# Performance work log

Hardware: AMD Instinct MI355X
Metric: run time of the kernel (lower is better)

## Reference

```python
import jax, jax.numpy as jnp
import numpy as np
from jax import lax

# physiological constants from the source module
DT = 1.0
TAU_L = 10.0
G_B = 0.6
G_L = 1.0 / TAU_L
LAMBDA_MAX = 0.35
STEPS = int(50 / DT)

IN_SIZE, HID, OUT, BATCH = 1024, 2048, 512, 4096


def setup_inputs() -> dict:
    key = jax.random.key(0)
    k1, k2, k3, k4, k5, k6 = jax.random.split(key, 6)
    psp = jax.random.uniform(k1, (IN_SIZE, BATCH), dtype=jnp.float32)  # |mm(spikes,kernel)| is >=0
    label = jax.random.uniform(k2, (BATCH, OUT), dtype=jnp.float32)    # teaching current I
    # Linear params init: uniform(-0.1, 0.1) as in the torch module
    W_h = jax.random.uniform(k3, (HID, IN_SIZE), minval=-0.1, maxval=0.1, dtype=jnp.float32)
    b_h = jax.random.uniform(k4, (HID,), minval=-0.1, maxval=0.1, dtype=jnp.float32)
    W_o = jax.random.uniform(k5, (OUT, HID), minval=-0.1, maxval=0.1, dtype=jnp.float32)
    b_o = jax.random.uniform(k6, (OUT,), minval=-0.1, maxval=0.1, dtype=jnp.float32)
    return {"psp": psp, "label": label, "W_h": W_h, "b_h": b_h, "W_o": W_o, "b_o": b_o}


def reference(psp, label, W_h, b_h, W_o, b_o):
    a = DT / TAU_L
    gr = G_B / G_L  # = 6.0
    x = psp.T  # [B, in] -- Hidden_layer transposes basal_input
    # psp is constant over the time loop, so the hidden basal GEMM hoists out
    basal_V_h = x @ W_h.T + b_h  # [B, HID]
    soma_h0 = jnp.zeros_like(basal_V_h)
    soma_o0 = jnp.zeros((x.shape[0], W_o.shape[0]), dtype=x.dtype)

    def step(carry, _):
        soma_h, soma_o = carry
        # hidden two-compartment leaky integration
        soma_h = soma_h + a * (-soma_h + gr * (basal_V_h - soma_h))
        rate_h = LAMBDA_MAX * jax.nn.sigmoid(soma_h)  # [B, HID]
        basal_V_o = rate_h @ W_o.T + b_o              # [B, OUT]
        # output layer, training (test=False) branch: nudged by teaching current I=label
        soma_o = soma_o + a * (-soma_o + gr * (basal_V_o - soma_o) + label - soma_o)
        return (soma_h, soma_o), None

    (soma_h, soma_o), _ = lax.scan(step, (soma_h0, soma_o0), None, length=STEPS)
    return LAMBDA_MAX * jax.nn.sigmoid(soma_o)  # out_layer.spike_rate, [B, OUT]
```

## Files before the change

kernel.cpp:

```cpp
#include <hip/hip_runtime.h>
#include <hip/hip_bf16.h>


typedef __bf16 bf16_t;
typedef __bf16 bf16x8 __attribute__((ext_vector_type(8)));
typedef __bf16 bf16x4v __attribute__((ext_vector_type(4)));
typedef float f32x4 __attribute__((ext_vector_type(4)));

#define GLD_TO_LDS16(gp, lp)                                            \
  __builtin_amdgcn_global_load_lds(                                     \
      (__attribute__((address_space(1))) void*)(void*)(gp),             \
      (__attribute__((address_space(3))) void*)(lp), 16, 0, 0)

__global__ __launch_bounds__(256) void transpose_cvt(
    const float* __restrict__ in, bf16_t* __restrict__ out, int R, int C) {
  __shared__ float tile[64][65];
  const int tx = threadIdx.x & 63;
  const int ty = threadIdx.x >> 6;
  const int r0 = blockIdx.y * 64;
  const int c0 = blockIdx.x * 64;
#pragma unroll
  for (int i = 0; i < 16; ++i) {
    const int r = ty + i * 4;
    tile[r][tx] = in[(size_t)(r0 + r) * C + c0 + tx];
  }
  __syncthreads();
#pragma unroll
  for (int i = 0; i < 16; ++i) {
    const int r = ty + i * 4;
    out[(size_t)(c0 + r) * R + r0 + tx] = (bf16_t)tile[tx][r];
  }
}

__global__ __launch_bounds__(256) void cvt2_f32_bf16(
    const float4* __restrict__ w1, bf16x4v* __restrict__ o1, int n1,
    const float4* __restrict__ w2, bf16x4v* __restrict__ o2, int n2) {
  const int i = blockIdx.x * 256 + threadIdx.x;
  const float4 v = (i < n1) ? w1[i] : w2[i - n1];
  bf16x4v o;
  o.x = (bf16_t)v.x; o.y = (bf16_t)v.y; o.z = (bf16_t)v.z; o.w = (bf16_t)v.w;
  if (i < n1) o1[i] = o;
  else if (i - n1 < n2) o2[i - n1] = o;
}

__global__ __launch_bounds__(256, 4) void gemm1_nt(
    const bf16_t* __restrict__ A, const bf16_t* __restrict__ Bt,
    const float* __restrict__ bias, bf16_t* __restrict__ C,
    int M, int N, int K) {
  constexpr int BK = 64;
  __shared__ __align__(16) bf16_t sA[128 * BK];
  __shared__ __align__(16) bf16_t sB[64 * BK];

  const int tid = threadIdx.x;
  const int wave = tid >> 6;
  const int lane = tid & 63;
  const int bm = blockIdx.x * 128;
  const int bn = blockIdx.y * 64;
  const int wm = (wave & 1) * 64;
  const int wn = (wave >> 1) * 32;

  f32x4 acc[4][2] = {};

  const int srow8 = lane >> 3;
  const int gseg = (lane & 7) ^ srow8;
  const bf16_t* Ag = A + (size_t)(bm + wave * 32 + srow8) * K + gseg * 8;
  const bf16_t* Bg = Bt + (size_t)(bn + wave * 16 + srow8) * K + gseg * 8;
  const int dstA = wave * 2048;
  const int dstB = wave * 1024;

  const int fr = lane & 15;
  const int qh = lane >> 4;

  for (int k0 = 0; k0 < K; k0 += BK) {
#pragma unroll
    for (int c = 0; c < 4; ++c)
      GLD_TO_LDS16(Ag + (size_t)(c * 8) * K + k0, sA + dstA + c * 512);
#pragma unroll
    for (int c = 0; c < 2; ++c)
      GLD_TO_LDS16(Bg + (size_t)(c * 8) * K + k0, sB + dstB + c * 512);
    __syncthreads();

#pragma unroll
    for (int ks = 0; ks < 2; ++ks) {
      const int q = ks * 4 + qh;
      bf16x8 av[4], bv[2];
#pragma unroll
      for (int i = 0; i < 4; ++i) {
        const int rr = wm + i * 16 + fr;
        av[i] = *(const bf16x8*)(sA + rr * BK + ((q ^ (rr & 7)) * 8));
      }
#pragma unroll
      for (int j = 0; j < 2; ++j) {
        const int rr = wn + j * 16 + fr;
        bv[j] = *(const bf16x8*)(sB + rr * BK + ((q ^ (rr & 7)) * 8));
      }
#pragma unroll
      for (int i = 0; i < 4; ++i)
#pragma unroll
        for (int j = 0; j < 2; ++j)
          acc[i][j] = __builtin_amdgcn_mfma_f32_16x16x32_bf16(
              av[i], bv[j], acc[i][j], 0, 0, 0);
    }
    __syncthreads();
  }

  const int cm0 = (lane >> 4) * 4;
#pragma unroll
  for (int j = 0; j < 2; ++j) {
    const int gn = bn + wn + j * 16 + fr;
    const float bj = bias[gn];
#pragma unroll
    for (int i = 0; i < 4; ++i) {
#pragma unroll
      for (int r = 0; r < 4; ++r) {
        const int gm = bm + wm + i * 16 + cm0 + r;
        const float z = 0.8571428571428571f * (acc[i][j][r] + bj);
        C[(size_t)gm * N + gn] = (bf16_t)(0.35f / (1.0f + __expf(-z)));
      }
    }
  }
}

__global__ __launch_bounds__(256, 4) void gemm2_nt(
    const bf16_t* __restrict__ A, const bf16_t* __restrict__ Bt,
    const float* __restrict__ bias, const float* __restrict__ lbl,
    float* __restrict__ out, int M, int N, int K) {
  constexpr int BK = 64;
  __shared__ __align__(16) bf16_t sA[32 * BK];
  __shared__ __align__(16) bf16_t sB[64 * BK];

  const int tid = threadIdx.x;
  const int wave = tid >> 6;
  const int lane = tid & 63;
  const int bm = blockIdx.x * 32;
  const int bn = blockIdx.y * 64;
  const int wm = (wave & 1) * 16;
  const int wn = (wave >> 1) * 32;

  f32x4 acc[2] = {};

  const int srow8 = lane >> 3;
  const int gseg = (lane & 7) ^ srow8;
  const bf16_t* Ag = A + (size_t)(bm + wave * 8 + srow8) * K + gseg * 8;
  const bf16_t* Bg = Bt + (size_t)(bn + wave * 16 + srow8) * K + gseg * 8;
  const int dstA = wave * 512;
  const int dstB = wave * 1024;

  const int fr = lane & 15;
  const int qh = lane >> 4;

  for (int k0 = 0; k0 < K; k0 += BK) {
    GLD_TO_LDS16(Ag + k0, sA + dstA);
#pragma unroll
    for (int c = 0; c < 2; ++c)
      GLD_TO_LDS16(Bg + (size_t)(c * 8) * K + k0, sB + dstB + c * 512);
    __syncthreads();

#pragma unroll
    for (int ks = 0; ks < 2; ++ks) {
      const int q = ks * 4 + qh;
      const int ra = wm + fr;
      const bf16x8 av =
          *(const bf16x8*)(sA + ra * BK + ((q ^ (ra & 7)) * 8));
      bf16x8 bv[2];
#pragma unroll
      for (int j = 0; j < 2; ++j) {
        const int rr = wn + j * 16 + fr;
        bv[j] = *(const bf16x8*)(sB + rr * BK + ((q ^ (rr & 7)) * 8));
      }
#pragma unroll
      for (int j = 0; j < 2; ++j)
        acc[j] = __builtin_amdgcn_mfma_f32_16x16x32_bf16(av, bv[j], acc[j],
                                                         0, 0, 0);
    }
    __syncthreads();
  }

  const int cm0 = (lane >> 4) * 4;
#pragma unroll
  for (int j = 0; j < 2; ++j) {
    const int gn = bn + wn + j * 16 + fr;
    const float bj = bias[gn];
#pragma unroll
    for (int r = 0; r < 4; ++r) {
      const int gm = bm + wm + cm0 + r;
      const float z =
          0.75f * (acc[j][r] + bj) + 0.125f * lbl[(size_t)gm * N + gn];
      out[(size_t)gm * N + gn] = 0.35f / (1.0f + __expf(-z));
    }
  }
}

extern "C" void kernel_launch(void* const* d_in, const int* in_sizes, int n_in,
                              void* d_out, int out_size, void* d_ws, size_t ws_size,
                              hipStream_t stream) {
  constexpr int IN = 1024, HID = 2048, OUT = 512, B = 4096;
  const float* psp = (const float*)d_in[0];
  const float* lbl = (const float*)d_in[1];
  const float* W_h = (const float*)d_in[2];
  const float* b_h = (const float*)d_in[3];
  const float* W_o = (const float*)d_in[4];
  const float* b_o = (const float*)d_in[5];
  float* out = (float*)d_out;

  bf16_t* Whb = (bf16_t*)d_ws;
  bf16_t* Wob = Whb + (size_t)HID * IN;
  bf16_t* pspT = Wob + (size_t)OUT * HID;
  bf16_t* Rm = pspT + (size_t)B * IN;

  transpose_cvt<<<dim3(B / 64, IN / 64), 256, 0, stream>>>(psp, pspT, IN, B);
  {
    const int n1 = HID * IN / 4, n2 = OUT * HID / 4;
    cvt2_f32_bf16<<<(n1 + n2 + 255) / 256, 256, 0, stream>>>(
        (const float4*)W_h, (bf16x4v*)Whb, n1,
        (const float4*)W_o, (bf16x4v*)Wob, n2);
  }
  gemm1_nt<<<dim3(B / 128, HID / 64), 256, 0, stream>>>(
      pspT, Whb, b_h, Rm, B, HID, IN);
  gemm2_nt<<<dim3(B / 32, OUT / 64), 256, 0, stream>>>(
      Rm, Wob, b_o, lbl, out, B, OUT, HID);
}
```

Before: 134.5 us.

## Load GEMM B operands straight to registers and merge prep kernels into one

Both GEMMs now read the weight (B) fragments directly from global memory into registers in MFMA operand layout, instead of staging them through LDS. This removes the B shared-memory tiles and their LDS reads. The psp transpose/convert and the weight bf16 conversion are merged into a single 1024-block prep kernel, which saves one launch. In exchange, each B load is a strided 16-byte-per-lane global access issued right before the barrier. Waves that share columns load the same B data twice, so the code relies on cache hits and exposes more global latency in the K loop.

```diff
diff --git a/kernel.cpp b/kernel.cpp
--- a/kernel.cpp
+++ b/kernel.cpp
@@ -12,35 +12,38 @@
       (__attribute__((address_space(1))) void*)(void*)(gp),             \
       (__attribute__((address_space(3))) void*)(lp), 16, 0, 0)
 
-__global__ __launch_bounds__(256) void transpose_cvt(
-    const float* __restrict__ in, bf16_t* __restrict__ out, int R, int C) {
+__global__ __launch_bounds__(256) void prep(
+    const float* __restrict__ psp, bf16_t* __restrict__ pspT,
+    const float4* __restrict__ w1, bf16x4v* __restrict__ o1, int n1,
+    const float4* __restrict__ w2, bf16x4v* __restrict__ o2, int n2) {
   __shared__ float tile[64][65];
-  const int tx = threadIdx.x & 63;
-  const int ty = threadIdx.x >> 6;
-  const int r0 = blockIdx.y * 64;
-  const int c0 = blockIdx.x * 64;
+  const int tid = threadIdx.x;
+  const int b = blockIdx.x;
+  const int c0 = (b & 63) * 64;
+  const int r0 = (b >> 6) * 64;
+  const int tx = tid & 63;
+  const int ty = tid >> 6;
 #pragma unroll
   for (int i = 0; i < 16; ++i) {
     const int r = ty + i * 4;
-    tile[r][tx] = in[(size_t)(r0 + r) * C + c0 + tx];
+    tile[r][tx] = psp[(size_t)(r0 + r) * 4096 + c0 + tx];
+  }
+  const int base = b * 768 + tid;
+#pragma unroll
+  for (int i = 0; i < 3; ++i) {
+    const int idx = base + i * 256;
+    const float4 v = (idx < n1) ? w1[idx] : w2[idx - n1];
+    bf16x4v o;
+    o.x = (bf16_t)v.x; o.y = (bf16_t)v.y; o.z = (bf16_t)v.z; o.w = (bf16_t)v.w;
+    if (idx < n1) o1[idx] = o;
+    else if (idx - n1 < n2) o2[idx - n1] = o;
   }
   __syncthreads();
 #pragma unroll
   for (int i = 0; i < 16; ++i) {
     const int r = ty + i * 4;
-    out[(size_t)(c0 + r) * R + r0 + tx] = (bf16_t)tile[tx][r];
-  }
-}
-
-__global__ __launch_bounds__(256) void cvt2_f32_bf16(
-    const float4* __restrict__ w1, bf16x4v* __restrict__ o1, int n1,
-    const float4* __restrict__ w2, bf16x4v* __restrict__ o2, int n2) {
-  const int i = blockIdx.x * 256 + threadIdx.x;
-  const float4 v = (i < n1) ? w1[i] : w2[i - n1];
-  bf16x4v o;
-  o.x = (bf16_t)v.x; o.y = (bf16_t)v.y; o.z = (bf16_t)v.z; o.w = (bf16_t)v.w;
-  if (i < n1) o1[i] = o;
-  else if (i - n1 < n2) o2[i - n1] = o;
+    pspT[(size_t)(c0 + r) * 1024 + r0 + tx] = (bf16_t)tile[tx][r];
+  }
 }
 
 __global__ __launch_bounds__(256, 4) void gemm1_nt(
@@ -49,7 +52,6 @@
     int M, int N, int K) {
   constexpr int BK = 64;
   __shared__ __align__(16) bf16_t sA[128 * BK];
-  __shared__ __align__(16) bf16_t sB[64 * BK];
 
   const int tid = threadIdx.x;
   const int wave = tid >> 6;
@@ -64,42 +66,39 @@
   const int srow8 = lane >> 3;
   const int gseg = (lane & 7) ^ srow8;
   const bf16_t* Ag = A + (size_t)(bm + wave * 32 + srow8) * K + gseg * 8;
-  const bf16_t* Bg = Bt + (size_t)(bn + wave * 16 + srow8) * K + gseg * 8;
   const int dstA = wave * 2048;
-  const int dstB = wave * 1024;
 
   const int fr = lane & 15;
   const int qh = lane >> 4;
+  const bf16_t* Bj0 = Bt + (size_t)(bn + wn + fr) * K + qh * 8;
+  const bf16_t* Bj1 = Bj0 + (size_t)16 * K;
 
   for (int k0 = 0; k0 < K; k0 += BK) {
 #pragma unroll
     for (int c = 0; c < 4; ++c)
       GLD_TO_LDS16(Ag + (size_t)(c * 8) * K + k0, sA + dstA + c * 512);
-#pragma unroll
-    for (int c = 0; c < 2; ++c)
-      GLD_TO_LDS16(Bg + (size_t)(c * 8) * K + k0, sB + dstB + c * 512);
+    bf16x8 bv[2][2];
+    bv[0][0] = *(const bf16x8*)(Bj0 + k0);
+    bv[0][1] = *(const bf16x8*)(Bj1 + k0);
+    bv[1][0] = *(const bf16x8*)(Bj0 + k0 + 32);
+    bv[1][1] = *(const bf16x8*)(Bj1 + k0 + 32);
     __syncthreads();
 
 #pragma unroll
     for (int ks = 0; ks < 2; ++ks) {
       const int q = ks * 4 + qh;
-      bf16x8 av[4], bv[2];
+      bf16x8 av[4];
 #pragma unroll
       for (int i = 0; i < 4; ++i) {
         const int rr = wm + i * 16 + fr;
         av[i] = *(const bf16x8*)(sA + rr * BK + ((q ^ (rr & 7)) * 8));
       }
 #pragma unroll
-      for (int j = 0; j < 2; ++j) {
-        const int rr = wn + j * 16 + fr;
-        bv[j] = *(const bf16x8*)(sB + rr * BK + ((q ^ (rr & 7)) * 8));
-      }
-#pragma unroll
       for (int i = 0; i < 4; ++i)
 #pragma unroll
         for (int j = 0; j < 2; ++j)
           acc[i][j] = __builtin_amdgcn_mfma_f32_16x16x32_bf16(
-              av[i], bv[j], acc[i][j], 0, 0, 0);
+              av[i], bv[ks][j], acc[i][j], 0, 0, 0);
     }
     __syncthreads();
   }
@@ -127,7 +126,6 @@
     float* __restrict__ out, int M, int N, int K) {
   constexpr int BK = 64;
   __shared__ __align__(16) bf16_t sA[32 * BK];
-  __shared__ __align__(16) bf16_t sB[64 * BK];
 
   const int tid = threadIdx.x;
   const int wave = tid >> 6;
@@ -142,36 +140,31 @@
   const int srow8 = lane >> 3;
   const int gseg = (lane & 7) ^ srow8;
   const bf16_t* Ag = A + (size_t)(bm + wave * 8 + srow8) * K + gseg * 8;
-  const bf16_t* Bg = Bt + (size_t)(bn + wave * 16 + srow8) * K + gseg * 8;
   const int dstA = wave * 512;
-  const int dstB = wave * 1024;
 
   const int fr = lane & 15;
   const int qh = lane >> 4;
+  const bf16_t* Bj0 = Bt + (size_t)(bn + wn + fr) * K + qh * 8;
+  const bf16_t* Bj1 = Bj0 + (size_t)16 * K;
 
   for (int k0 = 0; k0 < K; k0 += BK) {
     GLD_TO_LDS16(Ag + k0, sA + dstA);
-#pragma unroll
-    for (int c = 0; c < 2; ++c)
-      GLD_TO_LDS16(Bg + (size_t)(c * 8) * K + k0, sB + dstB + c * 512);
+    bf16x8 bv[2][2];
+    bv[0][0] = *(const bf16x8*)(Bj0 + k0);
+    bv[0][1] = *(const bf16x8*)(Bj1 + k0);
+    bv[1][0] = *(const bf16x8*)(Bj0 + k0 + 32);
+    bv[1][1] = *(const bf16x8*)(Bj1 + k0 + 32);
     __syncthreads();
 
 #pragma unroll
     for (int ks = 0; ks < 2; ++ks) {
       const int q = ks * 4 + qh;
       const int ra = wm + fr;
-      const bf16x8 av =
-          *(const bf16x8*)(sA + ra * BK + ((q ^ (ra & 7)) * 8));
-      bf16x8 bv[2];
-#pragma unroll
-      for (int j = 0; j < 2; ++j) {
-        const int rr = wn + j * 16 + fr;
-        bv[j] = *(const bf16x8*)(sB + rr * BK + ((q ^ (rr & 7)) * 8));
-      }
+      const bf16x8 av = *(const bf16x8*)(sA + ra * BK + ((q ^ (ra & 7)) * 8));
 #pragma unroll
       for (int j = 0; j < 2; ++j)
-        acc[j] = __builtin_amdgcn_mfma_f32_16x16x32_bf16(av, bv[j], acc[j],
-                                                         0, 0, 0);
+        acc[j] = __builtin_amdgcn_mfma_f32_16x16x32_bf16(av, bv[ks][j],
+                                                         acc[j], 0, 0, 0);
     }
     __syncthreads();
   }
@@ -208,13 +201,9 @@
   bf16_t* pspT = Wob + (size_t)OUT * HID;
   bf16_t* Rm = pspT + (size_t)B * IN;
 
-  transpose_cvt<<<dim3(B / 64, IN / 64), 256, 0, stream>>>(psp, pspT, IN, B);
-  {
-    const int n1 = HID * IN / 4, n2 = OUT * HID / 4;
-    cvt2_f32_bf16<<<(n1 + n2 + 255) / 256, 256, 0, stream>>>(
-        (const float4*)W_h, (bf16x4v*)Whb, n1,
-        (const float4*)W_o, (bf16x4v*)Wob, n2);
-  }
+  prep<<<1024, 256, 0, stream>>>(
+      psp, pspT, (const float4*)W_h, (bf16x4v*)Whb, HID * IN / 4,
+      (const float4*)W_o, (bf16x4v*)Wob, OUT * HID / 4);
   gemm1_nt<<<dim3(B / 128, HID / 64), 256, 0, stream>>>(
       pspT, Whb, b_h, Rm, B, HID, IN);
   gemm2_nt<<<dim3(B / 32, OUT / 64), 256, 0, stream>>>(
```

Measured after the change: 195.9 us. 1.46x slower.
